# Kernel tuning notes

Measured on AMD Instinct MI355X. Metric: run time of the kernel, lower is better.

## Reference

```python
import jax, jax.numpy as jnp
import numpy as np

B, C, H, W = 16, 192, 56, 56   # feature map from visual encoder
K = 9                          # kNN neighbors (knn_graph k)
NUM_CLASSES = 100
PRED_DIM = 1024                # pred_emb_dim
EPS = 1e-5                     # BatchNorm eps


def setup_inputs() -> dict:
    key = jax.random.key(0)
    ks = jax.random.split(key, 6)
    def kaiming(k, shape, fan_in):
        return jax.random.normal(k, shape, jnp.float32) * np.float32(np.sqrt(2.0 / fan_in))
    return {
        "image_feature_map": jax.random.normal(ks[0], (B, C, H, W), jnp.float32),
        # 1x1 conv patch-prediction head: Conv2d(C, NUM_CLASSES, 1)
        "conv_w": kaiming(ks[1], (NUM_CLASSES, C), C),
        "conv_b": jnp.zeros((NUM_CLASSES,), jnp.float32),
        # stand-in for opaque GSAT GNN: one linear + mean neighbor aggregation
        "gnn_w": kaiming(ks[2], (C, C), C),
        "gnn_b": jnp.zeros((C,), jnp.float32),
        # prediction head: Linear(C, PRED_DIM) -> BN -> GELU -> Linear(PRED_DIM, NUM_CLASSES)
        "w1": kaiming(ks[3], (C, PRED_DIM), C),
        "b1": jnp.zeros((PRED_DIM,), jnp.float32),
        "bn_gamma": jnp.ones((PRED_DIM,), jnp.float32),
        "bn_beta": jnp.zeros((PRED_DIM,), jnp.float32),
        "w2": kaiming(ks[4], (PRED_DIM, NUM_CLASSES), PRED_DIM),
        "b2": jnp.zeros((NUM_CLASSES,), jnp.float32),
    }


def _knn_edges(x_norm):
    """x_norm: [B, N, C] L2-normalized. Per-image kNN (no cross-batch edges,
    no self loops). Returns global (src, dst) of shape [B*N*K] each,
    src = neighbor, dst = center node (PyG source_to_target flow)."""
    N = x_norm.shape[1]
    # normalized vectors: argmin Euclidean dist == argmax cosine sim
    sim = jnp.einsum('bnc,bmc->bnm', x_norm, x_norm)          # [B,N,N]
    sim = sim - 4.0 * jnp.eye(N, dtype=sim.dtype)             # exclude self
    _, nbr = jax.lax.top_k(sim, K)                            # [B,N,K]
    offs = (jnp.arange(B) * N)[:, None, None]
    src = (nbr + offs).reshape(-1)
    dst = (jnp.broadcast_to(jnp.arange(N)[None, :, None], (B, N, K)) + offs).reshape(-1)
    return src, dst


def reference(image_feature_map, conv_w, conv_b, gnn_w, gnn_b,
              w1, b1, bn_gamma, bn_beta, w2, b2):
    N = H * W
    # patch predictions: 1x1 conv over feature map
    patch_pred = jnp.einsum('bchw,kc->bkhw', image_feature_map, conv_w) + conv_b[None, :, None, None]
    # reshape_into_graph_input: [B,C,H,W] -> [B*N, C] nodes, then L2 normalize
    x = image_feature_map.reshape(B, C, N).transpose(0, 2, 1)  # [B,N,C]
    x = x / jnp.maximum(jnp.linalg.norm(x, axis=-1, keepdims=True), 1e-12)
    # knn_graph under no_grad
    src, dst = _knn_edges(jax.lax.stop_gradient(x))
    nodes = x.reshape(B * N, C)
    # GNN stand-in: linear + relu, edge attention, mean neighbor aggregation
    h = jax.nn.relu(nodes @ gnn_w + gnn_b)                     # [B*N, C]
    raw_edge_att = jnp.sum(h[src] * h[dst], axis=-1)           # [B*N*K]
    edge_att = jax.nn.sigmoid(raw_edge_att)
    msg = jax.ops.segment_sum(h[src], dst, num_segments=B * N)
    h = h + msg / np.float32(K)
    # global_add_pool over batch assignment
    batch = jnp.repeat(jnp.arange(B), N)
    g = jax.ops.segment_sum(h, batch, num_segments=B)          # [B, C]
    # prediction MLP: Linear -> BatchNorm1d (train-mode batch stats) -> GELU -> Linear
    z = g @ w1 + b1
    mu = jnp.mean(z, axis=0)
    var = jnp.var(z, axis=0)
    z = (z - mu) * jax.lax.rsqrt(var + EPS) * bn_gamma + bn_beta
    z = jax.nn.gelu(z, approximate=False)
    pred = z @ w2 + b2                                         # [B, NUM_CLASSES]
    return (pred, edge_att, patch_pred)
```

## Files before the change

kernel.cpp:

```cpp
#include <hip/hip_runtime.h>
#include <math.h>

#define B_  16
#define C_  192
#define N_  3136
#define BN_ 50176
#define K_  9
#define NC_ 100
#define PD_ 1024
#define NSEV 7
#define SEVCOLS 448

#define OUT_EATT 1600
#define OUT_PP   453184

typedef short bf16x8 __attribute__((ext_vector_type(8)));
typedef float f32x16 __attribute__((ext_vector_type(16)));

__device__ __forceinline__ unsigned int umaxu(unsigned int a, unsigned int b) { return a > b ? a : b; }
__device__ __forceinline__ unsigned int uminu(unsigned int a, unsigned int b) { return a < b ? a : b; }
__device__ __forceinline__ unsigned int med3u(unsigned int a, unsigned int b, unsigned int c) {
    unsigned int d;
    asm("v_med3_u32 %0, %1, %2, %3" : "=v"(d) : "v"(a), "v"(b), "v"(c));
    return d;
}
__device__ __forceinline__ void ins12m(unsigned int (&lk)[12], unsigned int key) {
    unsigned int nk[12];
    nk[0] = umaxu(lk[0], key);
    #pragma unroll
    for (int k = 1; k < 12; ++k) nk[k] = med3u(lk[k - 1], lk[k], key);
    #pragma unroll
    for (int k = 0; k < 12; ++k) lk[k] = nk[k];
}

template<int NL>
__device__ inline void ins_lex(float (&lv)[NL], int (&li)[NL], float v, int vi) {
    if (v > lv[NL-1] || (v == lv[NL-1] && vi < li[NL-1])) {
        #pragma unroll
        for (int k = 0; k < NL; ++k) {
            bool p = (v > lv[k]) || (v == lv[k] && vi < li[k]);
            float fv = p ? lv[k] : v; int fi = p ? li[k] : vi;
            lv[k] = p ? v : lv[k];    li[k] = p ? vi : li[k];
            v = fv; vi = fi;
        }
    }
}

__device__ inline unsigned int bf16_rne(unsigned int u) {
    return (u + 0x7fffu + ((u >> 16) & 1u)) & 0xffff0000u;
}

__global__ __launch_bounds__(256) void k_normalize(const float* __restrict__ in,
        float* __restrict__ xn, unsigned short* __restrict__ xsn,
        float* __restrict__ norms) {
    __shared__ float tile[C_][65];
    __shared__ float part[4][64];
    __shared__ float rnorm_s[64];
    int b = blockIdx.x & 15;
    int n0 = (blockIdx.x >> 4) * 64;
    int t = threadIdx.x;
    for (int f = t; f < C_ * 64; f += 256) {
        int c = f >> 6, n = f & 63;
        tile[c][n] = in[((size_t)b * C_ + c) * N_ + n0 + n];
    }
    __syncthreads();
    {
        int n = t & 63, qq = t >> 6;
        float s = 0.f;
        #pragma unroll
        for (int i = 0; i < 48; ++i) { float v = tile[qq * 48 + i][n]; s += v * v; }
        part[qq][n] = s;
    }
    __syncthreads();
    if (t < 64) {
        float tot = part[0][t] + part[1][t] + part[2][t] + part[3][t];
        float nrm = fmaxf(sqrtf(tot), 1e-12f);
        norms[(size_t)b * N_ + n0 + t] = nrm;
        rnorm_s[t] = 1.0f / nrm;
    }
    __syncthreads();
    for (int f = t; f < 64 * 96; f += 256) {
        int n = f / 96, cp = f - n * 96;
        int c = cp * 2;
        float r = rnorm_s[n];
        float v0 = tile[c][n] * r;
        float v1 = tile[c + 1][n] * r;
        size_t row = (size_t)b * N_ + n0 + n;
        *(float2*)(xn + row * C_ + c) = make_float2(v0, v1);
        unsigned int h0 = bf16_rne(__float_as_uint(v0));
        unsigned int h1 = bf16_rne(__float_as_uint(v1));
        unsigned int l0 = bf16_rne(__float_as_uint(v0 - __uint_as_float(h0)));
        unsigned int l1 = bf16_rne(__float_as_uint(v1 - __uint_as_float(h1)));
        unsigned int* xr = (unsigned int*)(xsn + row * 384);
        xr[cp]      = (h0 >> 16) | (h1 & 0xffff0000u);
        xr[96 + cp] = (l0 >> 16) | (l1 & 0xffff0000u);
    }
}

__global__ __launch_bounds__(256) void k_wsplit(const float* __restrict__ cw,
        const float* __restrict__ gw, const float* __restrict__ w2,
        unsigned short* __restrict__ wsc, unsigned short* __restrict__ wsg,
        float* __restrict__ w2t) {
    int id = blockIdx.x * 256 + threadIdx.x;
    if (id < 128 * 192) {
        int k = id / 192, c = id - k * 192;
        float v = (k < 100) ? cw[k * 192 + c] : 0.f;
        unsigned int h = bf16_rne(__float_as_uint(v));
        wsc[(size_t)k * 384 + c] = (unsigned short)(h >> 16);
        wsc[(size_t)k * 384 + 192 + c] =
            (unsigned short)(bf16_rne(__float_as_uint(v - __uint_as_float(h))) >> 16);
    } else if (id < 61440) {
        int e = id - 128 * 192;
        int cc = e / 192, j = e - cc * 192;
        float v = gw[cc * 192 + j];
        unsigned int h = bf16_rne(__float_as_uint(v));
        wsg[(size_t)j * 384 + cc] = (unsigned short)(h >> 16);
        wsg[(size_t)j * 384 + 192 + cc] =
            (unsigned short)(bf16_rne(__float_as_uint(v - __uint_as_float(h))) >> 16);
    } else {
        int e2 = id - 61440;
        int jj = e2 >> 10, k = e2 & 1023;
        w2t[(size_t)jj * PD_ + k] = w2[(size_t)k * NC_ + jj];
    }
}

#define STAGE32(DST, SRCBASE, NLW) { \
    const char* s_ = (SRCBASE); \
    _Pragma("unroll") \
    for (int q_ = 0; q_ < NLW; ++q_) \
        __builtin_amdgcn_global_load_lds( \
            (const __attribute__((address_space(1))) unsigned int*)(s_ + q_ * 32), \
            (__attribute__((address_space(3))) unsigned int*)((DST) + (w * NLW + q_) * 1024), 16, 0, 0); }

#define STAGEHALF(DST, COLB, KH) { \
    const char* s_ = xsi + (size_t)((COLB) + l31) * 768 + (KH) * 384 + w * 96 + lh * 16; \
    _Pragma("unroll") \
    for (int q_ = 0; q_ < 3; ++q_) \
        __builtin_amdgcn_global_load_lds( \
            (const __attribute__((address_space(1))) unsigned int*)(s_ + q_ * 32), \
            (__attribute__((address_space(3))) unsigned int*)((DST) + (w * 3 + q_) * 1024), 16, 0, 0); }

#define SCAN16 { \
    int c0 = cbase + c * 32 + 4 * lh; \
    int selfslot = r - c0; \
    int kc = 4095 - c0; \
    _Pragma("unroll") \
    for (int g = 0; g < 4; ++g) { \
        _Pragma("unroll") \
        for (int q = 0; q < 4; ++q) { \
            unsigned int u = __float_as_uint(fmaf(acc[4 * g + q], 0.125f, 0.75f)); \
            unsigned int key = ((u >> 3) << 12) | (unsigned int)(kc - (8 * g + q)); \
            key = (8 * g + q == selfslot) ? 0u : key; \
            ins12m(lk, key); \
        } \
    } }

__global__ __launch_bounds__(256, 3) void k_simmfma(const unsigned short* __restrict__ xs,
        unsigned int* __restrict__ topk) {
    __shared__ __align__(1024) char SMEM[24576];
    int bid = blockIdx.x;
    int img = bid & 15;
    int rest = bid >> 4;
    int rb = rest / NSEV;
    int sv = rest - rb * NSEV;
    int t = threadIdx.x;
    int w = t >> 6, lane = t & 63;
    int l31 = lane & 31, lh = lane >> 5;
    const char* xsi = (const char*)(xs + (size_t)img * N_ * 384);

    int r = rb * 128 + w * 32 + l31;
    bool valid = r < N_;
    int rl = valid ? r : (N_ - 1);
    bf16x8 bfrag[24];
    {
        const char* rp = xsi + (size_t)rl * 768 + lh * 16;
        #pragma unroll
        for (int ks = 0; ks < 24; ++ks)
            bfrag[ks] = *(const bf16x8*)(rp + ks * 32);
    }
    unsigned int lk[12];
    #pragma unroll
    for (int k = 0; k < 12; ++k) lk[k] = 0u;

    int cbase = sv * SEVCOLS;

    STAGEHALF(SMEM, cbase, 0)
    __syncthreads();

    for (int c = 0; c < 14; ++c) {
        STAGEHALF(SMEM + 12288, cbase + c * 32, 1)
        f32x16 acc;
        #pragma unroll
        for (int i = 0; i < 16; ++i) acc[i] = 0.f;
        {
            const char* rp = SMEM + lh * 512 + l31 * 16;
            #pragma unroll
            for (int ks = 0; ks < 12; ++ks) {
                bf16x8 af = *(const bf16x8*)(rp + ks * 1024);
                acc = __builtin_amdgcn_mfma_f32_32x32x16_bf16(af, bfrag[ks], acc, 0, 0, 0);
            }
        }
        __syncthreads();
        if (c < 13) { STAGEHALF(SMEM, cbase + (c + 1) * 32, 0) }
        {
            const char* rp = SMEM + 12288 + lh * 512 + l31 * 16;
            #pragma unroll
            for (int ks = 0; ks < 12; ++ks) {
                bf16x8 af = *(const bf16x8*)(rp + ks * 1024);
                acc = __builtin_amdgcn_mfma_f32_32x32x16_bf16(af, bfrag[12 + ks], acc, 0, 0, 0);
            }
        }
        if (valid) SCAN16
        __syncthreads();
    }
    unsigned int pk[12];
    #pragma unroll
    for (int j = 0; j < 12; ++j)
        pk[j] = (unsigned int)__shfl_xor((int)lk[j], 32, 64);
    #pragma unroll
    for (int j = 0; j < 12; ++j) ins12m(lk, pk[j]);
    if (valid && lh == 0) {
        unsigned int* op = topk + ((size_t)sv * BN_ + (size_t)img * N_ + r) * 12;
        #pragma unroll
        for (int k = 0; k < 12; ++k) op[k] = lk[k];
    }
}

__global__ __launch_bounds__(256, 3) void k_patchmfma(const unsigned short* __restrict__ xs,
        const unsigned short* __restrict__ wsc, const float* __restrict__ norms,
        const float* __restrict__ cb, float* __restrict__ outp) {
    __shared__ __align__(1024) char SMEM[49152];
    int bid = blockIdx.x;
    int img = bid & 15;
    int n0 = (bid >> 4) * 64;
    int t = threadIdx.x;
    int w = t >> 6, lane = t & 63;
    int l31 = lane & 31, lh = lane >> 5;
    const char* xsi = (const char*)(xs + (size_t)img * N_ * 384);
    int ch = w * 32 + l31;
    bf16x8 bfrag[24];
    {
        const char* wp = (const char*)wsc + (size_t)ch * 768 + lh * 16;
        #pragma unroll
        for (int ks = 0; ks < 24; ++ks)
            bfrag[ks] = *(const bf16x8*)(wp + ks * 32);
    }
    float bias = (ch < NC_) ? cb[ch] : 0.f;
    STAGE32(SMEM, xsi + (size_t)(n0 + l31) * 768 + w * 192 + lh * 16, 6);
    __syncthreads();
    for (int c = 0; c < 2; ++c) {
        char* cur = SMEM + (c & 1) * 24576;
        if (c == 0)
            STAGE32(SMEM + 24576, xsi + (size_t)(n0 + 32 + l31) * 768 + w * 192 + lh * 16, 6);
        f32x16 acc;
        #pragma unroll
        for (int i = 0; i < 16; ++i) acc[i] = 0.f;
        const char* rp = cur + lh * 512 + l31 * 16;
        #pragma unroll
        for (int ks = 0; ks < 24; ++ks) {
            bf16x8 af = *(const bf16x8*)(rp + ks * 1024);
            acc = __builtin_amdgcn_mfma_f32_32x32x16_bf16(af, bfrag[ks], acc, 0, 0, 0);
        }
        if (ch < NC_) {
            int nb = n0 + c * 32 + 4 * lh;
            float* op = outp + ((size_t)(img * NC_ + ch)) * N_ + nb;
            const float* npv = norms + (size_t)img * N_ + nb;
            #pragma unroll
            for (int g = 0; g < 4; ++g) {
                float4 nv = *(const float4*)(npv + 8 * g);
                float4 o;
                o.x = acc[4 * g + 0] * nv.x + bias;
                o.y = acc[4 * g + 1] * nv.y + bias;
                o.z = acc[4 * g + 2] * nv.z + bias;
                o.w = acc[4 * g + 3] * nv.w + bias;
                *(float4*)(op + 8 * g) = o;
            }
        }
        __syncthreads();
    }
}

__global__ __launch_bounds__(384, 3) void k_gnnmfma(const unsigned short* __restrict__ xs,
        const unsigned short* __restrict__ wsg, const float* __restrict__ gbias,
        float* __restrict__ h) {
    __shared__ __align__(1024) char SMEM[49152];
    int n0 = blockIdx.x * 128;
    int t = threadIdx.x;
    int w = t / 64, lane = t & 63;
    int l31 = lane & 31, lh = lane >> 5;
    int j = w * 32 + l31;
    bf16x8 bfrag[24];
    {
        const char* wp = (const char*)wsg + (size_t)j * 768 + lh * 16;
        #pragma unroll
        for (int ks = 0; ks < 24; ++ks)
            bfrag[ks] = *(const bf16x8*)(wp + ks * 32);
    }
    float bj = gbias[j];
    STAGE32(SMEM, (const char*)xs + (size_t)(n0 + l31) * 768 + w * 128 + lh * 16, 4);
    __syncthreads();
    for (int c = 0; c < 4; ++c) {
        char* cur = SMEM + (c & 1) * 24576;
        if (c < 3) {
            char* dst = SMEM + ((c & 1) ^ 1) * 24576;
            STAGE32(dst, (const char*)xs + (size_t)(n0 + (c + 1) * 32 + l31) * 768 + w * 128 + lh * 16, 4);
        }
        f32x16 acc;
        #pragma unroll
        for (int i = 0; i < 16; ++i) acc[i] = 0.f;
        const char* rp = cur + lh * 512 + l31 * 16;
        #pragma unroll
        for (int ks = 0; ks < 24; ++ks) {
            bf16x8 af = *(const bf16x8*)(rp + ks * 1024);
            acc = __builtin_amdgcn_mfma_f32_32x32x16_bf16(af, bfrag[ks], acc, 0, 0, 0);
        }
        int nb = n0 + c * 32 + 4 * lh;
        #pragma unroll
        for (int g = 0; g < 4; ++g)
            #pragma unroll
            for (int q = 0; q < 4; ++q)
                h[(size_t)(nb + 8 * g + q) * C_ + j] = fmaxf(acc[4 * g + q] + bj, 0.f);
        __syncthreads();
    }
}

__global__ __launch_bounds__(256) void k_merge2(const unsigned int* __restrict__ topk,
        int* __restrict__ nbr12) {
    int row = blockIdx.x * 256 + threadIdx.x;
    unsigned int lk[12];
    const unsigned int* p0 = topk + (size_t)row * 12;
    #pragma unroll
    for (int k = 0; k < 12; ++k) lk[k] = p0[k];
    #pragma unroll
    for (int h = 1; h < NSEV; ++h) {
        const unsigned int* p1 = topk + ((size_t)h * BN_ + row) * 12;
        #pragma unroll
        for (int j = 0; j < 12; ++j) ins12m(lk, p1[j]);
    }
    int gb = (row / N_) * N_;
    int* np = nbr12 + (size_t)row * 12;
    #pragma unroll
    for (int k = 0; k < 12; ++k) np[k] = gb + (4095 - (int)(lk[k] & 0xFFFu));
}

__global__ __launch_bounds__(256) void k_rescore(const float* __restrict__ xn,
        const int* __restrict__ nbr12, int* __restrict__ nbr9) {
    int img = blockIdx.x & 15;
    int sub = blockIdx.x >> 4;
    int t = threadIdx.x;
    int lane = t & 63;
    int row = img * N_ + sub * 16 + (t >> 4);
    int c = lane & 15;
    int cand = nbr12[(size_t)row * 12 + (c < 12 ? c : 0)];
    const float4* xa = (const float4*)(xn + (size_t)row * C_);
    const float4* xb = (const float4*)(xn + (size_t)cand * C_);
    float dot = 0.f;
    #pragma unroll
    for (int k = 0; k < 48; ++k) {
        float4 p = xa[k], q = xb[k];
        dot += p.x*q.x + p.y*q.y + p.z*q.z + p.w*q.w;
    }
    float v = (c < 12 && cand != row) ? dot : -1e30f;
    float lv[9]; int li[9];
    #pragma unroll
    for (int k = 0; k < 9; ++k) { lv[k] = -1e30f; li[k] = 0x7fffffff; }
    int gbase = lane & 48;
    #pragma unroll
    for (int j = 0; j < 12; ++j) {
        float vj = __shfl(v, gbase + j, 64);
        int  ij = __shfl(cand, gbase + j, 64);
        ins_lex<9>(lv, li, vj, ij);
    }
    if (c == 0) {
        int* np = nbr9 + (size_t)row * 9;
        #pragma unroll
        for (int k = 0; k < 9; ++k) np[k] = li[k];
    }
}

__global__ __launch_bounds__(256) void k_edge(const float* __restrict__ h,
        const int* __restrict__ nbr, float* __restrict__ eatt,
        float* __restrict__ gparte) {
    __shared__ float ps[4][C_];
    int img = blockIdx.x & 15;
    int sub = blockIdx.x >> 4;
    int ng = threadIdx.x >> 6;
    int node = img * N_ + sub * 4 + ng;
    int lane = threadIdx.x & 63;
    const float* hc = h + (size_t)node * C_;
    float c0 = hc[lane], c1 = hc[lane + 64], c2 = hc[lane + 128];
    float m0 = 0.f, m1 = 0.f, m2 = 0.f;
    const int* np_ = nbr + (size_t)node * K_;
    float* ep = eatt + (size_t)node * K_;
    #pragma unroll
    for (int k = 0; k < K_; ++k) {
        int src = np_[k];
        const float* hs = h + (size_t)src * C_;
        float s0 = hs[lane], s1 = hs[lane + 64], s2 = hs[lane + 128];
        float d = c0 * s0 + c1 * s1 + c2 * s2;
        d += __shfl_xor(d, 1, 64);  d += __shfl_xor(d, 2, 64);
        d += __shfl_xor(d, 4, 64);  d += __shfl_xor(d, 8, 64);
        d += __shfl_xor(d, 16, 64); d += __shfl_xor(d, 32, 64);
        if (lane == 0) ep[k] = 1.0f / (1.0f + expf(-d));
        m0 += s0; m1 += s1; m2 += s2;
    }
    const float r9 = 1.0f / 9.0f;
    ps[ng][lane]       = c0 + m0 * r9;
    ps[ng][lane + 64]  = c1 + m1 * r9;
    ps[ng][lane + 128] = c2 + m2 * r9;
    __syncthreads();
    if (threadIdx.x < C_) {
        int ch = threadIdx.x;
        gparte[(size_t)blockIdx.x * C_ + ch] =
            (ps[0][ch] + ps[1][ch]) + (ps[2][ch] + ps[3][ch]);
    }
}

__global__ __launch_bounds__(192) void k_gred(const float* __restrict__ gparte,
        float* __restrict__ gpart) {
    int b = blockIdx.x >> 3, s = blockIdx.x & 7;
    int oc = threadIdx.x;
    float acc = 0.f;
    for (int sub = s * 98; sub < (s + 1) * 98; ++sub)
        acc += gparte[((size_t)(sub * 16 + b)) * C_ + oc];
    gpart[(size_t)blockIdx.x * C_ + oc] = acc;
}

__global__ __launch_bounds__(256) void k_mlp1(const float* __restrict__ gpart,
        const float* __restrict__ w1, const float* __restrict__ b1,
        const float* __restrict__ gam, const float* __restrict__ bet,
        float* __restrict__ zs) {
    __shared__ float gs[B_ * C_];
    int t = threadIdx.x;
    int j = blockIdx.x * 256 + t;
    for (int f = t; f < B_ * C_; f += 256) {
        int b = f / C_, oc = f - b * C_;
        float a = 0.f;
        #pragma unroll
        for (int s = 0; s < 8; ++s) a += gpart[((size_t)b * 8 + s) * C_ + oc];
        gs[f] = a;
    }
    __syncthreads();
    float z[16];
    #pragma unroll
    for (int i = 0; i < 16; ++i) z[i] = b1[j];
    for (int c = 0; c < C_; ++c) {
        float w = w1[(size_t)c * PD_ + j];
        #pragma unroll
        for (int i = 0; i < 16; ++i) z[i] += gs[i * C_ + c] * w;
    }
    float mu = 0.f;
    #pragma unroll
    for (int i = 0; i < 16; ++i) mu += z[i];
    mu *= (1.0f / 16.0f);
    float var = 0.f;
    #pragma unroll
    for (int i = 0; i < 16; ++i) { float d = z[i] - mu; var += d * d; }
    var *= (1.0f / 16.0f);
    float sc = (1.0f / sqrtf(var + 1e-5f)) * gam[j];
    float bt = bet[j];
    #pragma unroll
    for (int i = 0; i < 16; ++i) {
        float zh = (z[i] - mu) * sc + bt;
        zs[(size_t)i * PD_ + j] = 0.5f * zh * (1.0f + erff(zh * 0.70710678118654752f));
    }
}

__global__ __launch_bounds__(64) void k_mlp2(const float* __restrict__ zs,
        const float* __restrict__ w2t, const float* __restrict__ b2,
        float* __restrict__ pred) {
    int i = blockIdx.x / NC_, jj = blockIdx.x - i * NC_;
    int lane = threadIdx.x;
    const float* zr = zs + (size_t)i * PD_;
    const float* wr = w2t + (size_t)jj * PD_;
    float a = 0.f;
    #pragma unroll
    for (int k = 0; k < 16; ++k) a += zr[lane + 64 * k] * wr[lane + 64 * k];
    a += __shfl_xor(a, 1, 64);  a += __shfl_xor(a, 2, 64);
    a += __shfl_xor(a, 4, 64);  a += __shfl_xor(a, 8, 64);
    a += __shfl_xor(a, 16, 64); a += __shfl_xor(a, 32, 64);
    if (lane == 0) pred[i * NC_ + jj] = a + b2[jj];
}

extern "C" void kernel_launch(void* const* d_in, const int* in_sizes, int n_in,
                              void* d_out, int out_size, void* d_ws, size_t ws_size,
                              hipStream_t stream) {
    const float* img    = (const float*)d_in[0];
    const float* conv_w = (const float*)d_in[1];
    const float* conv_b = (const float*)d_in[2];
    const float* gnn_w  = (const float*)d_in[3];
    const float* gnn_b  = (const float*)d_in[4];
    const float* w1     = (const float*)d_in[5];
    const float* b1     = (const float*)d_in[6];
    const float* bng    = (const float*)d_in[7];
    const float* bnb    = (const float*)d_in[8];
    const float* w2     = (const float*)d_in[9];
    const float* b2     = (const float*)d_in[10];
    float* out = (float*)d_out;

    float* XN            = (float*)d_ws;
    unsigned short* XS   = (unsigned short*)(XN + (size_t)BN_ * C_);
    unsigned int* TOPK   = (unsigned int*)(XS + (size_t)BN_ * 384);
    int*   NBR12         = (int*)(TOPK + (size_t)NSEV * BN_ * 12);
    int*   NBR9          = NBR12 + (size_t)BN_ * 12;
    float* NORMS         = (float*)(NBR9 + (size_t)BN_ * K_);
    unsigned short* WSC  = (unsigned short*)(NORMS + BN_);
    unsigned short* WSG  = WSC + (size_t)128 * 384;
    float* GPART         = (float*)(WSG + (size_t)192 * 384);
    float* W2T           = GPART + (size_t)128 * C_;
    float* Hh            = XN;
    float* GPARTE        = (float*)TOPK;
    float* ZS            = (float*)NBR12;

    k_normalize<<<784, 256, 0, stream>>>(img, XN, XS, NORMS);
    k_wsplit   <<<640, 256, 0, stream>>>(conv_w, gnn_w, w2, WSC, WSG, W2T);
    k_patchmfma<<<784, 256, 0, stream>>>(XS, WSC, NORMS, conv_b, out + OUT_PP);
    k_simmfma  <<<2800, 256, 0, stream>>>(XS, TOPK);
    k_merge2   <<<196, 256, 0, stream>>>(TOPK, NBR12);
    k_rescore  <<<3136, 256, 0, stream>>>(XN, NBR12, NBR9);
    k_gnnmfma  <<<392, 384, 0, stream>>>(XS, WSG, gnn_b, Hh);
    k_edge     <<<12544, 256, 0, stream>>>(Hh, NBR9, out + OUT_EATT, GPARTE);
    k_gred     <<<128, 192, 0, stream>>>(GPARTE, GPART);
    k_mlp1     <<<4, 256, 0, stream>>>(GPART, w1, b1, bng, bnb, ZS);
    k_mlp2     <<<1600, 64, 0, stream>>>(ZS, W2T, b2, out);
}
```

Before: 429.6 us.

## Vectorize edge kernel, halve patch LDS, add MFMA priority, shrink reductions

The edge-attention kernel now gives each node 16 lanes with float4 loads instead of a full wave with scalar loads, so each block handles 16 nodes. This reduces the grid fourfold and shortens the shuffle reductions. The partial-sum reduction kernel is resized to match: 4 splits of 49 instead of 8 of 98, and mlp1 sums 4 partials. The patch-conv kernel switches to half-K staging with 24KB of LDS, which may allow more blocks per CU. The similarity kernel wraps its MFMA loops in s_setprio to favour matrix work over other waves.

Measured after the change: 416.1 us. -3.1%, faster.

```diff
diff --git a/kernel.cpp b/kernel.cpp
--- a/kernel.cpp
+++ b/kernel.cpp
@@ -18,7 +18,6 @@
 typedef float f32x16 __attribute__((ext_vector_type(16)));
 
 __device__ __forceinline__ unsigned int umaxu(unsigned int a, unsigned int b) { return a > b ? a : b; }
-__device__ __forceinline__ unsigned int uminu(unsigned int a, unsigned int b) { return a < b ? a : b; }
 __device__ __forceinline__ unsigned int med3u(unsigned int a, unsigned int b, unsigned int c) {
     unsigned int d;
     asm("v_med3_u32 %0, %1, %2, %3" : "=v"(d) : "v"(a), "v"(b), "v"(c));
@@ -132,13 +131,13 @@
             (const __attribute__((address_space(1))) unsigned int*)(s_ + q_ * 32), \
             (__attribute__((address_space(3))) unsigned int*)((DST) + (w * NLW + q_) * 1024), 16, 0, 0); }
 
-#define STAGEHALF(DST, COLB, KH) { \
-    const char* s_ = xsi + (size_t)((COLB) + l31) * 768 + (KH) * 384 + w * 96 + lh * 16; \
+#define STAGEHALF(DST, BASE, COLB, KH, NLW) { \
     _Pragma("unroll") \
-    for (int q_ = 0; q_ < 3; ++q_) \
+    for (int q_ = 0; q_ < NLW; ++q_) { \
+        const char* s_ = (BASE) + (size_t)((COLB) + l31) * 768 + (KH) * 384 + (w * (NLW) + q_) * 32 + lh * 16; \
         __builtin_amdgcn_global_load_lds( \
-            (const __attribute__((address_space(1))) unsigned int*)(s_ + q_ * 32), \
-            (__attribute__((address_space(3))) unsigned int*)((DST) + (w * 3 + q_) * 1024), 16, 0, 0); }
+            (const __attribute__((address_space(1))) unsigned int*)s_, \
+            (__attribute__((address_space(3))) unsigned int*)((DST) + (w * (NLW) + q_) * 1024), 16, 0, 0); } }
 
 #define SCAN16 { \
     int c0 = cbase + c * 32 + 4 * lh; \
@@ -184,31 +183,35 @@
 
     int cbase = sv * SEVCOLS;
 
-    STAGEHALF(SMEM, cbase, 0)
+    STAGEHALF(SMEM, xsi, cbase, 0, 3)
     __syncthreads();
 
     for (int c = 0; c < 14; ++c) {
-        STAGEHALF(SMEM + 12288, cbase + c * 32, 1)
+        STAGEHALF(SMEM + 12288, xsi, cbase + c * 32, 1, 3)
         f32x16 acc;
         #pragma unroll
         for (int i = 0; i < 16; ++i) acc[i] = 0.f;
         {
             const char* rp = SMEM + lh * 512 + l31 * 16;
+            __builtin_amdgcn_s_setprio(1);
             #pragma unroll
             for (int ks = 0; ks < 12; ++ks) {
                 bf16x8 af = *(const bf16x8*)(rp + ks * 1024);
                 acc = __builtin_amdgcn_mfma_f32_32x32x16_bf16(af, bfrag[ks], acc, 0, 0, 0);
             }
+            __builtin_amdgcn_s_setprio(0);
         }
         __syncthreads();
-        if (c < 13) { STAGEHALF(SMEM, cbase + (c + 1) * 32, 0) }
+        if (c < 13) { STAGEHALF(SMEM, xsi, cbase + (c + 1) * 32, 0, 3) }
         {
             const char* rp = SMEM + 12288 + lh * 512 + l31 * 16;
+            __builtin_amdgcn_s_setprio(1);
             #pragma unroll
             for (int ks = 0; ks < 12; ++ks) {
                 bf16x8 af = *(const bf16x8*)(rp + ks * 1024);
                 acc = __builtin_amdgcn_mfma_f32_32x32x16_bf16(af, bfrag[12 + ks], acc, 0, 0, 0);
             }
+            __builtin_amdgcn_s_setprio(0);
         }
         if (valid) SCAN16
         __syncthreads();
@@ -229,7 +232,7 @@
 __global__ __launch_bounds__(256, 3) void k_patchmfma(const unsigned short* __restrict__ xs,
         const unsigned short* __restrict__ wsc, const float* __restrict__ norms,
         const float* __restrict__ cb, float* __restrict__ outp) {
-    __shared__ __align__(1024) char SMEM[49152];
+    __shared__ __align__(1024) char SMEM[24576];
     int bid = blockIdx.x;
     int img = bid & 15;
     int n0 = (bid >> 4) * 64;
@@ -246,20 +249,30 @@
             bfrag[ks] = *(const bf16x8*)(wp + ks * 32);
     }
     float bias = (ch < NC_) ? cb[ch] : 0.f;
-    STAGE32(SMEM, xsi + (size_t)(n0 + l31) * 768 + w * 192 + lh * 16, 6);
+    STAGEHALF(SMEM, xsi, n0, 0, 3)
     __syncthreads();
     for (int c = 0; c < 2; ++c) {
-        char* cur = SMEM + (c & 1) * 24576;
-        if (c == 0)
-            STAGE32(SMEM + 24576, xsi + (size_t)(n0 + 32 + l31) * 768 + w * 192 + lh * 16, 6);
+        STAGEHALF(SMEM + 12288, xsi, n0 + c * 32, 1, 3)
         f32x16 acc;
         #pragma unroll
         for (int i = 0; i < 16; ++i) acc[i] = 0.f;
-        const char* rp = cur + lh * 512 + l31 * 16;
-        #pragma unroll
-        for (int ks = 0; ks < 24; ++ks) {
-            bf16x8 af = *(const bf16x8*)(rp + ks * 1024);
-            acc = __builtin_amdgcn_mfma_f32_32x32x16_bf16(af, bfrag[ks], acc, 0, 0, 0);
+        {
+            const char* rp = SMEM + lh * 512 + l31 * 16;
+            #pragma unroll
+            for (int ks = 0; ks < 12; ++ks) {
+                bf16x8 af = *(const bf16x8*)(rp + ks * 1024);
+                acc = __builtin_amdgcn_mfma_f32_32x32x16_bf16(af, bfrag[ks], acc, 0, 0, 0);
+            }
+        }
+        __syncthreads();
+        if (c == 0) { STAGEHALF(SMEM, xsi, n0 + 32, 0, 3) }
+        {
+            const char* rp = SMEM + 12288 + lh * 512 + l31 * 16;
+            #pragma unroll
+            for (int ks = 0; ks < 12; ++ks) {
+                bf16x8 af = *(const bf16x8*)(rp + ks * 1024);
+                acc = __builtin_amdgcn_mfma_f32_32x32x16_bf16(af, bfrag[12 + ks], acc, 0, 0, 0);
+            }
         }
         if (ch < NC_) {
             int nb = n0 + c * 32 + 4 * lh;
@@ -384,46 +397,67 @@
     __shared__ float ps[4][C_];
     int img = blockIdx.x & 15;
     int sub = blockIdx.x >> 4;
-    int ng = threadIdx.x >> 6;
-    int node = img * N_ + sub * 4 + ng;
-    int lane = threadIdx.x & 63;
-    const float* hc = h + (size_t)node * C_;
-    float c0 = hc[lane], c1 = hc[lane + 64], c2 = hc[lane + 128];
-    float m0 = 0.f, m1 = 0.f, m2 = 0.f;
+    int t = threadIdx.x;
+    int wv = t >> 6;
+    int nl = t >> 4;
+    int l16 = t & 15;
+    int node = img * N_ + sub * 16 + nl;
+    const float4* hc = (const float4*)(h + (size_t)node * C_) + l16;
+    float4 c0 = hc[0], c1 = hc[16], c2 = hc[32];
+    float4 m0 = make_float4(0,0,0,0), m1 = make_float4(0,0,0,0), m2 = make_float4(0,0,0,0);
     const int* np_ = nbr + (size_t)node * K_;
     float* ep = eatt + (size_t)node * K_;
     #pragma unroll
     for (int k = 0; k < K_; ++k) {
         int src = np_[k];
-        const float* hs = h + (size_t)src * C_;
-        float s0 = hs[lane], s1 = hs[lane + 64], s2 = hs[lane + 128];
-        float d = c0 * s0 + c1 * s1 + c2 * s2;
-        d += __shfl_xor(d, 1, 64);  d += __shfl_xor(d, 2, 64);
-        d += __shfl_xor(d, 4, 64);  d += __shfl_xor(d, 8, 64);
-        d += __shfl_xor(d, 16, 64); d += __shfl_xor(d, 32, 64);
-        if (lane == 0) ep[k] = 1.0f / (1.0f + expf(-d));
-        m0 += s0; m1 += s1; m2 += s2;
+        const float4* hs = (const float4*)(h + (size_t)src * C_) + l16;
+        float4 s0 = hs[0], s1 = hs[16], s2 = hs[32];
+        float d = s0.x*c0.x + s0.y*c0.y + s0.z*c0.z + s0.w*c0.w
+                + s1.x*c1.x + s1.y*c1.y + s1.z*c1.z + s1.w*c1.w
+                + s2.x*c2.x + s2.y*c2.y + s2.z*c2.z + s2.w*c2.w;
+        d += __shfl_xor(d, 1, 64);
+        d += __shfl_xor(d, 2, 64);
+        d += __shfl_xor(d, 4, 64);
+        d += __shfl_xor(d, 8, 64);
+        if (l16 == 0) ep[k] = 1.0f / (1.0f + expf(-d));
+        m0.x += s0.x; m0.y += s0.y; m0.z += s0.z; m0.w += s0.w;
+        m1.x += s1.x; m1.y += s1.y; m1.z += s1.z; m1.w += s1.w;
+        m2.x += s2.x; m2.y += s2.y; m2.z += s2.z; m2.w += s2.w;
     }
     const float r9 = 1.0f / 9.0f;
-    ps[ng][lane]       = c0 + m0 * r9;
-    ps[ng][lane + 64]  = c1 + m1 * r9;
-    ps[ng][lane + 128] = c2 + m2 * r9;
-    __syncthreads();
-    if (threadIdx.x < C_) {
-        int ch = threadIdx.x;
-        gparte[(size_t)blockIdx.x * C_ + ch] =
-            (ps[0][ch] + ps[1][ch]) + (ps[2][ch] + ps[3][ch]);
-    }
+    float v[12];
+    v[0] = c0.x + m0.x * r9; v[1]  = c0.y + m0.y * r9;
+    v[2] = c0.z + m0.z * r9; v[3]  = c0.w + m0.w * r9;
+    v[4] = c1.x + m1.x * r9; v[5]  = c1.y + m1.y * r9;
+    v[6] = c1.z + m1.z * r9; v[7]  = c1.w + m1.w * r9;
+    v[8] = c2.x + m2.x * r9; v[9]  = c2.y + m2.y * r9;
+    v[10] = c2.z + m2.z * r9; v[11] = c2.w + m2.w * r9;
+    #pragma unroll
+    for (int e = 0; e < 12; ++e) {
+        v[e] += __shfl_xor(v[e], 16, 64);
+        v[e] += __shfl_xor(v[e], 32, 64);
+    }
+    if ((t & 63) < 16) {
+        #pragma unroll
+        for (int j = 0; j < 3; ++j)
+            #pragma unroll
+            for (int e = 0; e < 4; ++e)
+                ps[wv][j * 64 + l16 * 4 + e] = v[j * 4 + e];
+    }
+    __syncthreads();
+    if (t < C_)
+        gparte[(size_t)blockIdx.x * C_ + t] =
+            (ps[0][t] + ps[1][t]) + (ps[2][t] + ps[3][t]);
 }
 
 __global__ __launch_bounds__(192) void k_gred(const float* __restrict__ gparte,
         float* __restrict__ gpart) {
-    int b = blockIdx.x >> 3, s = blockIdx.x & 7;
+    int b = blockIdx.x >> 2, s = blockIdx.x & 3;
     int oc = threadIdx.x;
     float acc = 0.f;
-    for (int sub = s * 98; sub < (s + 1) * 98; ++sub)
+    for (int sub = s * 49; sub < (s + 1) * 49; ++sub)
         acc += gparte[((size_t)(sub * 16 + b)) * C_ + oc];
-    gpart[(size_t)blockIdx.x * C_ + oc] = acc;
+    gpart[(size_t)(b * 4 + s) * C_ + oc] = acc;
 }
 
 __global__ __launch_bounds__(256) void k_mlp1(const float* __restrict__ gpart,
@@ -437,7 +471,7 @@
         int b = f / C_, oc = f - b * C_;
         float a = 0.f;
         #pragma unroll
-        for (int s = 0; s < 8; ++s) a += gpart[((size_t)b * 8 + s) * C_ + oc];
+        for (int s = 0; s < 4; ++s) a += gpart[((size_t)(b * 4 + s)) * C_ + oc];
         gs[f] = a;
     }
     __syncthreads();
@@ -519,8 +553,8 @@
     k_merge2   <<<196, 256, 0, stream>>>(TOPK, NBR12);
     k_rescore  <<<3136, 256, 0, stream>>>(XN, NBR12, NBR9);
     k_gnnmfma  <<<392, 384, 0, stream>>>(XS, WSG, gnn_b, Hh);
-    k_edge     <<<12544, 256, 0, stream>>>(Hh, NBR9, out + OUT_EATT, GPARTE);
-    k_gred     <<<128, 192, 0, stream>>>(GPARTE, GPART);
+    k_edge     <<<3136, 256, 0, stream>>>(Hh, NBR9, out + OUT_EATT, GPARTE);
+    k_gred     <<<64, 192, 0, stream>>>(GPARTE, GPART);
     k_mlp1     <<<4, 256, 0, stream>>>(GPART, w1, b1, bng, bnb, ZS);
     k_mlp2     <<<1600, 64, 0, stream>>>(ZS, W2T, b2, out);
 }
```
